# Performance work log

Hardware: AMD Instinct MI355X
Metric: run time of the kernel (lower is better)

## Reference

```python
import jax, jax.numpy as jnp
import numpy as np

B, S, D, H = 4, 2048, 1024, 1024  # batch, seq, input_dim, hidden_dim

def setup_inputs() -> dict:
    key = jax.random.key(0)
    k1, k2, k3, k4, k5 = jax.random.split(key, 5)
    scale1 = 1.0 / np.sqrt(D)
    scale2 = 1.0 / np.sqrt(H)
    return {
        "x": jax.random.normal(k1, (B, S, D), dtype=jnp.float32),
        "W1": jax.random.uniform(k2, (D, 3 * H), jnp.float32, -scale1, scale1),
        "b1": jax.random.uniform(k3, (3 * H,), jnp.float32, -scale1, scale1),
        "W2": jax.random.uniform(k4, (H, H), jnp.float32, -scale2, scale2),
        "b2": jax.random.uniform(k5, (H,), jnp.float32, -scale2, scale2),
    }

def reference(x, W1, b1, W2, b2):
    qkv = jnp.einsum('bsd,dh->bsh', x, W1) + b1          # [B,S,3H]
    q, k, v = jnp.split(qkv, 3, axis=-1)                  # each [B,S,H]
    scale = (2.0 * D) ** -0.5                             # faithful: (input_dim*2)^-0.5
    scores = jnp.einsum('bse,bSe->bsS', q, k) * scale     # [B,S,S]
    att = jax.nn.softmax(scores, axis=-1)
    ctx = jnp.einsum('bsS,bSe->bse', att, v)              # [B,S,H]
    out = jnp.einsum('bsh,hk->bsk', ctx, W2) + b2
    return out
```

## Files before the change

### kernel.cpp

```cpp
#include <hip/hip_runtime.h>
#include <hip/hip_bf16.h>
#include <stdint.h>

#define B_  4
#define S_  2048
#define D_  1024
#define H_  1024
#define BS_ (B_*S_)
#define N3H (3*H_)

typedef __bf16 bf16x8 __attribute__((ext_vector_type(8)));
typedef float  f32x4  __attribute__((ext_vector_type(4)));
typedef unsigned short u16x8 __attribute__((ext_vector_type(8)));

__device__ __forceinline__ unsigned short f2bf(float x) {
    unsigned u = __float_as_uint(x);
    return (unsigned short)((u + 0x7FFFu + ((u >> 16) & 1u)) >> 16);
}
__device__ __forceinline__ float bf2f(unsigned short h) {
    return __uint_as_float(((unsigned)h) << 16);
}

__device__ __forceinline__ void gload_lds16(const void* g, void* l) {
    __builtin_amdgcn_global_load_lds(
        (const __attribute__((address_space(1))) void*)g,
        (__attribute__((address_space(3))) void*)l, 16, 0, 0);
}

#define BAR __builtin_amdgcn_s_barrier()
#define DS_FENCE do { asm volatile("s_waitcnt lgkmcnt(0)" ::: "memory"); \
                      __builtin_amdgcn_sched_barrier(0); } while (0)

template<int EPI>
__global__ __launch_bounds__(512, 2) void gemm128(
    const unsigned short* __restrict__ A,
    const unsigned short* __restrict__ Bm,
    int NXt, int NYt, int N, int K,
    long long sAz, long long sBz, long long sOz,
    void* __restrict__ out0, void* __restrict__ out1, void* __restrict__ out2,
    const float* __restrict__ bias, float scale)
{
    __shared__ __align__(16) char lds[3 * 49152];

    const int nt_g = (int)gridDim.x;
    const int bid = (int)blockIdx.x;
    const int tile = (bid & 7) * (nt_g >> 3) + (bid >> 3);
    const int tx = tile % NXt;
    const int rest = tile / NXt;
    const int ty = rest % NYt;
    const int tz = rest / NYt;

    const unsigned short* Ab = A  + (long long)tz * sAz;
    const unsigned short* Bb = Bm + (long long)tz * sBz;
    const int rowBase = ty * 256;
    const int colBase = tx * 128;
    const int tid = threadIdx.x;
    const int w = tid >> 6, l = tid & 63;
    const int wr = w >> 2, wc = w & 3;
    const int fr = l & 15, fq = l >> 4;

    int sr[2], scl[2];
#pragma unroll
    for (int j = 0; j < 2; j++) {
        int o  = j * 8192 + tid * 16;
        int st = o >> 10;
        int wi = o & 1023;
        wi ^= ((wi >> 9) & 1) << 5;
        sr[j]  = (st >> 1) * 16 + (wi >> 6);
        scl[j] = (st & 1) * 32 + ((wi & 63) >> 1);
    }

    auto STAGE_A = [&](char* buf, int half, int t) {
        char* dst = buf + half * 16384 + w * 1024;
        const unsigned short* base =
            Ab + (long long)(rowBase + half * 128) * K + t * 64;
#pragma unroll
        for (int j = 0; j < 2; j++)
            gload_lds16(base + (long long)sr[j] * K + scl[j], dst + j * 8192);
    };
    auto STAGE_B = [&](char* buf, int half, int t) {
        char* dst = buf + 32768 + half * 8192 + w * 1024;
        const unsigned short* base =
            Bb + (long long)(colBase + half * 64) * K + t * 64;
        gload_lds16(base + (long long)sr[0] * K + scl[0], dst);
    };

    const int abase = (fr * 64 + fq * 16) ^ ((fr & 8) << 2);

#define MFMA82(AF, BF, MOFF) do { \
    __builtin_amdgcn_s_setprio(1); \
    _Pragma("unroll") for (int m_ = 0; m_ < 4; m_++) \
    _Pragma("unroll") for (int n_ = 0; n_ < 2; n_++) \
    _Pragma("unroll") for (int k_ = 0; k_ < 2; k_++) \
        acc[(MOFF)+m_][n_] = __builtin_amdgcn_mfma_f32_16x16x32_bf16( \
            AF[m_][k_], BF[n_][k_], acc[(MOFF)+m_][n_], 0, 0, 0); \
    __builtin_amdgcn_s_setprio(0); } while (0)

    f32x4 acc[8][2];
#pragma unroll
    for (int m = 0; m < 8; m++)
#pragma unroll
        for (int n = 0; n < 2; n++) acc[m][n] = (f32x4){0.f, 0.f, 0.f, 0.f};

    const int NT = K >> 6;

    STAGE_A(lds, 0, 0); STAGE_B(lds, 0, 0); STAGE_A(lds, 1, 0); STAGE_B(lds, 1, 0);
    STAGE_A(lds + 49152, 0, 1); STAGE_B(lds + 49152, 0, 1);
    STAGE_A(lds + 49152, 1, 1); STAGE_B(lds + 49152, 1, 1);
    asm volatile("s_waitcnt vmcnt(6)" ::: "memory");
    BAR;
    __builtin_amdgcn_sched_barrier(0);

    bf16x8 afA[4][2], afB[4][2], bf[2][2];

    for (int t = 0; t < NT; ++t) {
        const char* bc = lds + (t % 3) * 49152;
        char* bs = lds + ((t + 2) % 3) * 49152;
        int ts = t + 2; if (ts >= NT) ts -= NT;
        const char* Abw = bc + wr * 16384;
        const char* Bbw = bc + 32768 + (wc >> 1) * 8192 + (wc & 1) * 4096;

#pragma unroll
        for (int m = 0; m < 4; m++)
#pragma unroll
            for (int kk = 0; kk < 2; kk++)
                afA[m][kk] = *(const bf16x8*)(Abw + m * 2048 + kk * 1024 + abase);
#pragma unroll
        for (int n = 0; n < 2; n++)
#pragma unroll
            for (int kk = 0; kk < 2; kk++)
                bf[n][kk] = *(const bf16x8*)(Bbw + n * 2048 + kk * 1024 + abase);
        STAGE_A(bs, 0, ts); STAGE_B(bs, 0, ts);
        BAR; DS_FENCE;
        MFMA82(afA, bf, 0);
        BAR;

#pragma unroll
        for (int m = 0; m < 4; m++)
#pragma unroll
            for (int kk = 0; kk < 2; kk++)
                afB[m][kk] = *(const bf16x8*)(Abw + (m + 4) * 2048 + kk * 1024 + abase);
        STAGE_A(bs, 1, ts); STAGE_B(bs, 1, ts);
        BAR; DS_FENCE;
        MFMA82(afB, bf, 4);
        asm volatile("s_waitcnt vmcnt(6)" ::: "memory");
        BAR;
        __builtin_amdgcn_sched_barrier(0);
    }

    asm volatile("s_waitcnt vmcnt(0) lgkmcnt(0)" ::: "memory");

    const int crow0 = rowBase + wr * 128 + fq * 4;
    const int ccol0 = colBase + wc * 32 + fr;

#pragma unroll
    for (int n = 0; n < 2; n++) {
        const int col = ccol0 + n * 16;
        if constexpr (EPI == 0) {
            const float bv = bias[col];
            const int seg = col >> 10, scn = col & 1023;
            unsigned short* dst =
                (unsigned short*)(seg == 0 ? out0 : (seg == 1 ? out1 : out2));
#pragma unroll
            for (int m = 0; m < 8; m++) {
                const int r0 = crow0 + m * 16;
#pragma unroll
                for (int j = 0; j < 4; j++)
                    dst[(long long)(r0 + j) * 1024 + scn] = f2bf(acc[m][n][j] + bv);
            }
        } else if constexpr (EPI == 1) {
            unsigned short* dst = (unsigned short*)out0 + (long long)tz * sOz;
#pragma unroll
            for (int m = 0; m < 8; m++) {
                const int r0 = crow0 + m * 16;
#pragma unroll
                for (int j = 0; j < 4; j++)
                    dst[(long long)(r0 + j) * N + col] = f2bf(acc[m][n][j] * scale);
            }
        } else {
            float* dst = (float*)out0;
            const float bv = bias[col];
#pragma unroll
            for (int m = 0; m < 8; m++) {
                const int r0 = crow0 + m * 16;
#pragma unroll
                for (int j = 0; j < 4; j++)
                    dst[(long long)(r0 + j) * N + col] = acc[m][n][j] + bv;
            }
        }
    }
#undef MFMA82
}

template<int EPI>
__global__ __launch_bounds__(512, 2) void gemm256(
    const unsigned short* __restrict__ A,
    const unsigned short* __restrict__ Bm,
    int M, int N, int K,
    long long sAz, long long sBz, long long sOz,
    void* __restrict__ out0, void* __restrict__ out1, void* __restrict__ out2,
    const float* __restrict__ bias, float scale)
{
    __shared__ __align__(16) char lds[131072];
    (void)M;

    const unsigned short* Ab = A  + blockIdx.z * sAz;
    const unsigned short* Bb = Bm + blockIdx.z * sBz;
    const int rowBase = blockIdx.y * 256;
    const int colBase = blockIdx.x * 256;
    const int tid = threadIdx.x;
    const int w = tid >> 6, l = tid & 63;
    const int wr = w >> 2, wc = w & 3;
    const int fr = l & 15, fq = l >> 4;

    int sr[2], scl[2];
#pragma unroll
    for (int j = 0; j < 2; j++) {
        int o  = j * 8192 + tid * 16;
        int st = o >> 10;
        int wi = o & 1023;
        wi ^= ((wi >> 9) & 1) << 5;
        sr[j]  = (st >> 1) * 16 + (wi >> 6);
        scl[j] = (st & 1) * 32 + ((wi & 63) >> 1);
    }

    auto STAGE = [&](int buf, int which, int tile) {
        const unsigned short* mat = (which < 2) ? Ab : Bb;
        const int rt0 = ((which < 2) ? rowBase : colBase) + (which & 1) * 128;
        char* dst = lds + buf * 65536 + (which >> 1) * 32768
                        + (which & 1) * 16384 + w * 1024;
        const int k0 = tile * 64;
#pragma unroll
        for (int j = 0; j < 2; j++) {
            const unsigned short* src =
                mat + (long long)(rt0 + sr[j]) * K + k0 + scl[j];
            gload_lds16(src, dst + j * 8192);
        }
    };

    const int abase = (fr * 64 + fq * 16) ^ ((fr & 8) << 2);
    const char* Ah[2] = { lds + wr * 16384, lds + 65536 + wr * 16384 };
    const char* Bh[2] = { lds + 32768 + (wc >> 1) * 16384,
                          lds + 98304 + (wc >> 1) * 16384 };
    const int bn0 = (wc & 1) * 8192;

#define LA(b, m, kk) (*(const bf16x8*)(Ah[b] + (m)*2048 + (kk)*1024 + abase))
#define LB(b, n, kk) (*(const bf16x8*)(Bh[b] + bn0 + (n)*2048 + (kk)*1024 + abase))
#define MFMA16(AF, BF, MOFF, NOFF) do { \
    __builtin_amdgcn_s_setprio(1); \
    _Pragma("unroll") for (int m_ = 0; m_ < 4; m_++) \
    _Pragma("unroll") for (int n_ = 0; n_ < 2; n_++) \
    _Pragma("unroll") for (int k_ = 0; k_ < 2; k_++) \
        acc[(MOFF)+m_][(NOFF)+n_] = __builtin_amdgcn_mfma_f32_16x16x32_bf16( \
            AF[m_][k_], BF[n_][k_], acc[(MOFF)+m_][(NOFF)+n_], 0, 0, 0); \
    __builtin_amdgcn_s_setprio(0); } while (0)

    f32x4 acc[8][4];
#pragma unroll
    for (int m = 0; m < 8; m++)
#pragma unroll
        for (int n = 0; n < 4; n++) acc[m][n] = (f32x4){0.f, 0.f, 0.f, 0.f};

    const int NT = K >> 6;

    STAGE(0, 0, 0); STAGE(0, 1, 0); STAGE(0, 2, 0); STAGE(0, 3, 0);
    STAGE(1, 0, 1); STAGE(1, 1, 1);
    asm volatile("s_waitcnt vmcnt(4)" ::: "memory");
    BAR;
    __builtin_amdgcn_sched_barrier(0);

    bf16x8 afA[4][2], afB[4][2], bfA[2][2], bfB[2][2];

    for (int i = 0; i < NT / 2; i++) {
        const int t1 = 2 * i + 1;
        int t2 = 2 * i + 2; if (t2 >= NT) t2 -= NT;
        int t3 = 2 * i + 3; if (t3 >= NT) t3 -= NT;

#pragma unroll
        for (int m = 0; m < 4; m++) { afA[m][0] = LA(0, m, 0); afA[m][1] = LA(0, m, 1); }
#pragma unroll
        for (int n = 0; n < 2; n++) { bfA[n][0] = LB(0, n, 0); bfA[n][1] = LB(0, n, 1); }
        STAGE(1, 2, t1);
        BAR; DS_FENCE;
        MFMA16(afA, bfA, 0, 0);
        BAR;
#pragma unroll
        for (int m = 0; m < 4; m++) { afB[m][0] = LA(0, 4 + m, 0); afB[m][1] = LA(0, 4 + m, 1); }
        STAGE(1, 3, t1);
        BAR; DS_FENCE;
        MFMA16(afB, bfA, 4, 0);
        BAR;
#pragma unroll
        for (int n = 0; n < 2; n++) { bfB[n][0] = LB(0, 2 + n, 0); bfB[n][1] = LB(0, 2 + n, 1); }
        STAGE(0, 0, t2);
        BAR; DS_FENCE;
        MFMA16(afA, bfB, 0, 2);
        BAR;
        STAGE(0, 1, t2);
        BAR;
        MFMA16(afB, bfB, 4, 2);
        asm volatile("s_waitcnt vmcnt(4)" ::: "memory");
        BAR;
        __builtin_amdgcn_sched_barrier(0);

#pragma unroll
        for (int m = 0; m < 4; m++) { afA[m][0] = LA(1, m, 0); afA[m][1] = LA(1, m, 1); }
#pragma unroll
        for (int n = 0; n < 2; n++) { bfA[n][0] = LB(1, n, 0); bfA[n][1] = LB(1, n, 1); }
        STAGE(0, 2, t2);
        BAR; DS_FENCE;
        MFMA16(afA, bfA, 0, 0);
        BAR;
#pragma unroll
        for (int m = 0; m < 4; m++) { afB[m][0] = LA(1, 4 + m, 0); afB[m][1] = LA(1, 4 + m, 1); }
        STAGE(0, 3, t2);
        BAR; DS_FENCE;
        MFMA16(afB, bfA, 4, 0);
        BAR;
#pragma unroll
        for (int n = 0; n < 2; n++) { bfB[n][0] = LB(1, 2 + n, 0); bfB[n][1] = LB(1, 2 + n, 1); }
        STAGE(1, 0, t3);
        BAR; DS_FENCE;
        MFMA16(afA, bfB, 0, 2);
        BAR;
        STAGE(1, 1, t3);
        BAR;
        MFMA16(afB, bfB, 4, 2);
        asm volatile("s_waitcnt vmcnt(4)" ::: "memory");
        BAR;
        __builtin_amdgcn_sched_barrier(0);
    }

    asm volatile("s_waitcnt vmcnt(0) lgkmcnt(0)" ::: "memory");

    const int crow0 = rowBase + wr * 128 + fq * 4;
    const int ccol0 = colBase + wc * 64 + fr;

#pragma unroll
    for (int n = 0; n < 4; n++) {
        const int col = ccol0 + n * 16;
        if constexpr (EPI == 1) {
            unsigned short* dst = (unsigned short*)out0 + blockIdx.z * sOz;
#pragma unroll
            for (int m = 0; m < 8; m++) {
                const int r0 = crow0 + m * 16;
#pragma unroll
                for (int j = 0; j < 4; j++)
                    dst[(long long)(r0 + j) * N + col] = f2bf(acc[m][n][j] * scale);
            }
        }
    }
    (void)out1; (void)out2; (void)bias;
#undef LA
#undef LB
#undef MFMA16
}

__global__ __launch_bounds__(256) void conv_f32_bf16(
    const float* __restrict__ in, unsigned short* __restrict__ out, int n8)
{
    for (int i = blockIdx.x * blockDim.x + threadIdx.x; i < n8;
         i += gridDim.x * blockDim.x) {
        const float4 a = ((const float4*)in)[2 * i];
        const float4 b = ((const float4*)in)[2 * i + 1];
        u16x8 o;
        o[0] = f2bf(a.x); o[1] = f2bf(a.y); o[2] = f2bf(a.z); o[3] = f2bf(a.w);
        o[4] = f2bf(b.x); o[5] = f2bf(b.y); o[6] = f2bf(b.z); o[7] = f2bf(b.w);
        ((u16x8*)out)[i] = o;
    }
}

__global__ __launch_bounds__(256) void tconv_f32_bf16(
    const float* __restrict__ in, unsigned short* __restrict__ out,
    int rows, int cols)
{
    __shared__ float t[32][33];
    const int c0 = blockIdx.x * 32, r0 = blockIdx.y * 32;
    const int tx = threadIdx.x & 31, ty = threadIdx.x >> 5;
#pragma unroll
    for (int i = 0; i < 4; i++)
        t[ty + 8 * i][tx] = in[(long long)(r0 + ty + 8 * i) * cols + c0 + tx];
    __syncthreads();
#pragma unroll
    for (int i = 0; i < 4; i++)
        out[(long long)(c0 + ty + 8 * i) * rows + r0 + tx] = f2bf(t[tx][ty + 8 * i]);
}

__global__ __launch_bounds__(256) void t_bf16(
    const unsigned short* __restrict__ in, unsigned short* __restrict__ out,
    int rows, int cols, long long sIz, long long sOz)
{
    __shared__ unsigned short t[32][33];
    in  += blockIdx.z * sIz;
    out += blockIdx.z * sOz;
    const int c0 = blockIdx.x * 32, r0 = blockIdx.y * 32;
    const int tx = threadIdx.x & 31, ty = threadIdx.x >> 5;
#pragma unroll
    for (int i = 0; i < 4; i++)
        t[ty + 8 * i][tx] = in[(long long)(r0 + ty + 8 * i) * cols + c0 + tx];
    __syncthreads();
#pragma unroll
    for (int i = 0; i < 4; i++)
        out[(long long)(c0 + ty + 8 * i) * rows + r0 + tx] = t[tx][ty + 8 * i];
}

__global__ __launch_bounds__(256) void softmax_rows(unsigned short* __restrict__ sc)
{
    const long long row = blockIdx.x;
    unsigned short* p = sc + row * S_;
    const int tid = threadIdx.x, w = tid >> 6, l = tid & 63;

    u16x8 v = *reinterpret_cast<const u16x8*>(&p[tid * 8]);
    float f[8];
#pragma unroll
    for (int i = 0; i < 8; i++) f[i] = bf2f(v[i]);

    float m = f[0];
#pragma unroll
    for (int i = 1; i < 8; i++) m = fmaxf(m, f[i]);
    for (int o = 32; o; o >>= 1) m = fmaxf(m, __shfl_xor(m, o));
    __shared__ float red[8];
    if (l == 0) red[w] = m;
    __syncthreads();
    m = fmaxf(fmaxf(red[0], red[1]), fmaxf(red[2], red[3]));

    float s = 0.f;
#pragma unroll
    for (int i = 0; i < 8; i++) { f[i] = __expf(f[i] - m); s += f[i]; }
    for (int o = 32; o; o >>= 1) s += __shfl_xor(s, o);
    if (l == 0) red[4 + w] = s;
    __syncthreads();
    s = red[4] + red[5] + red[6] + red[7];

    const float inv = 1.0f / s;
    u16x8 o8;
#pragma unroll
    for (int i = 0; i < 8; i++) o8[i] = f2bf(f[i] * inv);
    *reinterpret_cast<u16x8*>(&p[tid * 8]) = o8;
}

extern "C" void kernel_launch(void* const* d_in, const int* in_sizes, int n_in,
                              void* d_out, int out_size, void* d_ws, size_t ws_size,
                              hipStream_t stream)
{
    (void)in_sizes; (void)n_in; (void)out_size; (void)ws_size;
    const float* x  = (const float*)d_in[0];
    const float* W1 = (const float*)d_in[1];
    const float* b1 = (const float*)d_in[2];
    const float* W2 = (const float*)d_in[3];
    const float* b2 = (const float*)d_in[4];
    float* out = (float*)d_out;

    char* ws = (char*)d_ws;
    size_t off = 0;
    auto alloc = [&](size_t bytes) {
        void* p = ws + off;
        off += (bytes + 255) & ~(size_t)255;
        return p;
    };
    unsigned short* xbf = (unsigned short*)alloc((size_t)BS_ * D_ * 2);
    unsigned short* w1t = (unsigned short*)alloc((size_t)N3H * D_ * 2);
    unsigned short* w2t = (unsigned short*)alloc((size_t)H_ * H_ * 2);
    unsigned short* q   = (unsigned short*)alloc((size_t)BS_ * H_ * 2);
    unsigned short* k   = (unsigned short*)alloc((size_t)BS_ * H_ * 2);
    unsigned short* v   = (unsigned short*)alloc((size_t)BS_ * H_ * 2);
    unsigned short* vt  = (unsigned short*)alloc((size_t)BS_ * H_ * 2);
    unsigned short* sc  = (unsigned short*)alloc((size_t)B_ * S_ * S_ * 2);
    unsigned short* ctx = v;

    const float scale = 0.022097086912079608f;

    conv_f32_bf16<<<dim3(2048), dim3(256), 0, stream>>>(x, xbf, BS_ * D_ / 8);
    tconv_f32_bf16<<<dim3(N3H / 32, D_ / 32), dim3(256), 0, stream>>>(W1, w1t, D_, N3H);
    tconv_f32_bf16<<<dim3(H_ / 32, H_ / 32), dim3(256), 0, stream>>>(W2, w2t, H_, H_);

    gemm128<0><<<dim3(768), dim3(512), 0, stream>>>(
        xbf, w1t, 24, 32, N3H, D_, 0LL, 0LL, 0LL, q, k, v, b1, 1.0f);

    t_bf16<<<dim3(H_ / 32, S_ / 32, B_), dim3(256), 0, stream>>>(
        v, vt, S_, H_, (long long)S_ * H_, (long long)S_ * H_);

    gemm256<1><<<dim3(S_ / 256, S_ / 256, B_), dim3(512), 0, stream>>>(
        q, k, S_, S_, H_, (long long)S_ * H_, (long long)S_ * H_, (long long)S_ * S_,
        sc, nullptr, nullptr, nullptr, scale);

    softmax_rows<<<dim3(BS_), dim3(256), 0, stream>>>(sc);

    gemm128<1><<<dim3(256), dim3(512), 0, stream>>>(
        sc, vt, 8, 8, H_, S_, (long long)S_ * S_, (long long)H_ * S_,
        (long long)S_ * H_, ctx, nullptr, nullptr, nullptr, 1.0f);

    gemm128<3><<<dim3(256), dim3(512), 0, stream>>>(
        ctx, w2t, 8, 32, H_, H_, 0LL, 0LL, 0LL, out, nullptr, nullptr, b2, 1.0f);
}
```

Before: 213.7 us.

## Reshape gemm128 warp tiling to 4x2 and regroup tile order per XCD

Changes the per-wave output tile in gemm128 from 128x32 to 64x64 (4 wave rows by 2 wave cols). The A fragments are now loaded once per k-step and reused across two B halves, so fewer LDS reads are spent per MFMA. It also remaps block-to-tile ordering within each XCD so that groups of 4 consecutive blocks cover row tiles sharing the same column, aiming at better L2 reuse. The remap assumes NXt and tile counts divide evenly; otherwise some tiles may be missed or duplicated.

```diff
diff --git a/kernel.cpp b/kernel.cpp
--- a/kernel.cpp
+++ b/kernel.cpp
@@ -44,11 +44,17 @@
 
     const int nt_g = (int)gridDim.x;
     const int bid = (int)blockIdx.x;
-    const int tile = (bid & 7) * (nt_g >> 3) + (bid >> 3);
+    const int C = nt_g >> 3;
+    const int c = bid >> 3;
+    const int xcd = bid & 7;
+    const int qq = c >> 2;
+    const int txl = qq % NXt;
+    const int rest = (c & 3) + 4 * (qq / NXt);
+    const int tile = xcd * C + rest * NXt + txl;
     const int tx = tile % NXt;
-    const int rest = tile / NXt;
-    const int ty = rest % NYt;
-    const int tz = rest / NYt;
+    const int rest2 = tile / NXt;
+    const int ty = rest2 % NYt;
+    const int tz = rest2 / NYt;
 
     const unsigned short* Ab = A  + (long long)tz * sAz;
     const unsigned short* Bb = Bm + (long long)tz * sBz;
@@ -56,7 +62,7 @@
     const int colBase = tx * 128;
     const int tid = threadIdx.x;
     const int w = tid >> 6, l = tid & 63;
-    const int wr = w >> 2, wc = w & 3;
+    const int wr = w >> 1, wc = w & 1;
     const int fr = l & 15, fq = l >> 4;
 
     int sr[2], scl[2];
@@ -87,20 +93,20 @@
 
     const int abase = (fr * 64 + fq * 16) ^ ((fr & 8) << 2);
 
-#define MFMA82(AF, BF, MOFF) do { \
+#define MFMA44(AF, BF, NOFF) do { \
     __builtin_amdgcn_s_setprio(1); \
     _Pragma("unroll") for (int m_ = 0; m_ < 4; m_++) \
     _Pragma("unroll") for (int n_ = 0; n_ < 2; n_++) \
     _Pragma("unroll") for (int k_ = 0; k_ < 2; k_++) \
-        acc[(MOFF)+m_][n_] = __builtin_amdgcn_mfma_f32_16x16x32_bf16( \
-            AF[m_][k_], BF[n_][k_], acc[(MOFF)+m_][n_], 0, 0, 0); \
+        acc[m_][(NOFF)+n_] = __builtin_amdgcn_mfma_f32_16x16x32_bf16( \
+            AF[m_][k_], BF[n_][k_], acc[m_][(NOFF)+n_], 0, 0, 0); \
     __builtin_amdgcn_s_setprio(0); } while (0)
 
-    f32x4 acc[8][2];
-#pragma unroll
-    for (int m = 0; m < 8; m++)
-#pragma unroll
-        for (int n = 0; n < 2; n++) acc[m][n] = (f32x4){0.f, 0.f, 0.f, 0.f};
+    f32x4 acc[4][4];
+#pragma unroll
+    for (int m = 0; m < 4; m++)
+#pragma unroll
+        for (int n = 0; n < 4; n++) acc[m][n] = (f32x4){0.f, 0.f, 0.f, 0.f};
 
     const int NT = K >> 6;
 
@@ -111,14 +117,14 @@
     BAR;
     __builtin_amdgcn_sched_barrier(0);
 
-    bf16x8 afA[4][2], afB[4][2], bf[2][2];
+    bf16x8 afA[4][2], bfA[2][2], bfB[2][2];
 
     for (int t = 0; t < NT; ++t) {
         const char* bc = lds + (t % 3) * 49152;
         char* bs = lds + ((t + 2) % 3) * 49152;
         int ts = t + 2; if (ts >= NT) ts -= NT;
-        const char* Abw = bc + wr * 16384;
-        const char* Bbw = bc + 32768 + (wc >> 1) * 8192 + (wc & 1) * 4096;
+        const char* Abw = bc + (wr >> 1) * 16384 + (wr & 1) * 8192;
+        const char* Bbw = bc + 32768 + wc * 8192;
 
 #pragma unroll
         for (int m = 0; m < 4; m++)
@@ -129,20 +135,20 @@
         for (int n = 0; n < 2; n++)
 #pragma unroll
             for (int kk = 0; kk < 2; kk++)
-                bf[n][kk] = *(const bf16x8*)(Bbw + n * 2048 + kk * 1024 + abase);
+                bfA[n][kk] = *(const bf16x8*)(Bbw + n * 2048 + kk * 1024 + abase);
         STAGE_A(bs, 0, ts); STAGE_B(bs, 0, ts);
         BAR; DS_FENCE;
-        MFMA82(afA, bf, 0);
-        BAR;
-
-#pragma unroll
-        for (int m = 0; m < 4; m++)
+        MFMA44(afA, bfA, 0);
+        BAR;
+
+#pragma unroll
+        for (int n = 0; n < 2; n++)
 #pragma unroll
             for (int kk = 0; kk < 2; kk++)
-                afB[m][kk] = *(const bf16x8*)(Abw + (m + 4) * 2048 + kk * 1024 + abase);
+                bfB[n][kk] = *(const bf16x8*)(Bbw + (n + 2) * 2048 + kk * 1024 + abase);
         STAGE_A(bs, 1, ts); STAGE_B(bs, 1, ts);
         BAR; DS_FENCE;
-        MFMA82(afB, bf, 4);
+        MFMA44(afA, bfB, 2);
         asm volatile("s_waitcnt vmcnt(6)" ::: "memory");
         BAR;
         __builtin_amdgcn_sched_barrier(0);
@@ -150,11 +156,11 @@
 
     asm volatile("s_waitcnt vmcnt(0) lgkmcnt(0)" ::: "memory");
 
-    const int crow0 = rowBase + wr * 128 + fq * 4;
-    const int ccol0 = colBase + wc * 32 + fr;
-
-#pragma unroll
-    for (int n = 0; n < 2; n++) {
+    const int crow0 = rowBase + wr * 64 + fq * 4;
+    const int ccol0 = colBase + wc * 64 + fr;
+
+#pragma unroll
+    for (int n = 0; n < 4; n++) {
         const int col = ccol0 + n * 16;
         if constexpr (EPI == 0) {
             const float bv = bias[col];
@@ -162,7 +168,7 @@
             unsigned short* dst =
                 (unsigned short*)(seg == 0 ? out0 : (seg == 1 ? out1 : out2));
 #pragma unroll
-            for (int m = 0; m < 8; m++) {
+            for (int m = 0; m < 4; m++) {
                 const int r0 = crow0 + m * 16;
 #pragma unroll
                 for (int j = 0; j < 4; j++)
@@ -171,7 +177,7 @@
         } else if constexpr (EPI == 1) {
             unsigned short* dst = (unsigned short*)out0 + (long long)tz * sOz;
 #pragma unroll
-            for (int m = 0; m < 8; m++) {
+            for (int m = 0; m < 4; m++) {
                 const int r0 = crow0 + m * 16;
 #pragma unroll
                 for (int j = 0; j < 4; j++)
@@ -181,7 +187,7 @@
             float* dst = (float*)out0;
             const float bv = bias[col];
 #pragma unroll
-            for (int m = 0; m < 8; m++) {
+            for (int m = 0; m < 4; m++) {
                 const int r0 = crow0 + m * 16;
 #pragma unroll
                 for (int j = 0; j < 4; j++)
@@ -189,7 +195,7 @@
             }
         }
     }
-#undef MFMA82
+#undef MFMA44
 }
 
 template<int EPI>
```

After: 206.4 us. 3.4% less time.
